# Optimization experiments

Hardware: AMD Instinct MI355X
Metric: run time of the kernel (lower is better)

## Reference

```python
import jax, jax.numpy as jnp
import numpy as np

B, S, D, H, F, E, K = 2, 2048, 1024, 16, 4096, 8, 2
EPS = 1e-6


def setup_inputs() -> dict:
    key = jax.random.key(0)
    ks = jax.random.split(key, 9)
    s = 0.02
    return {
        "x": jax.random.normal(ks[0], (B, S, D), jnp.float32),
        "n1_w": jnp.ones((D,), jnp.float32),
        "n2_w": jnp.ones((D,), jnp.float32),
        "wq": jax.random.normal(ks[1], (D, D), jnp.float32) * s,
        "wk": jax.random.normal(ks[2], (D, D), jnp.float32) * s,
        "wv": jax.random.normal(ks[3], (D, D), jnp.float32) * s,
        "wo": jax.random.normal(ks[4], (D, D), jnp.float32) * s,
        "router_w": jax.random.normal(ks[5], (E, D), jnp.float32) * s,  # nn.Linear(D, E, bias=False)
        "w1": jax.random.normal(ks[6], (E, D, F), jnp.float32) * s,
        "b1": jnp.zeros((E, F), jnp.float32),
        "w2": jax.random.normal(ks[7], (E, F, D), jnp.float32) * s,
        "b2": jnp.zeros((E, D), jnp.float32),
    }


def _rms(t, w):
    return t * w * jax.lax.rsqrt(jnp.mean(t * t, axis=-1, keepdims=True) + EPS)


def reference(x, n1_w, n2_w, wq, wk, wv, wo, router_w, w1, b1, w2, b2):
    hd = D // H
    # --- pre-norm causal multi-head self-attention ---
    h = _rms(x, n1_w)
    q = (h @ wq).reshape(B, S, H, hd)
    k = (h @ wk).reshape(B, S, H, hd)
    v = (h @ wv).reshape(B, S, H, hd)
    scores = jnp.einsum("bqhd,bkhd->bhqk", q, k) * (hd ** -0.5)
    causal = jnp.tril(jnp.ones((S, S), bool))
    scores = jnp.where(causal, scores, jnp.float32(-1e9))
    attn = jax.nn.softmax(scores, axis=-1)
    attn_out = jnp.einsum("bhqk,bkhd->bqhd", attn, v).reshape(B, S, D) @ wo
    x = x + attn_out
    # --- pre-norm MoE MLP: dense experts + top-k weighted combine ---
    h2 = _rms(x, n2_w)
    logits = h2 @ router_w.T                         # [B,S,E]
    probs = jax.nn.softmax(logits, axis=-1)
    topv, topi = jax.lax.top_k(probs, K)             # [B,S,K]
    topv = topv / jnp.sum(topv, axis=-1, keepdims=True)  # renormalized top-k gates
    bi = jnp.arange(B)[:, None, None]
    si = jnp.arange(S)[None, :, None]
    gates = jnp.zeros_like(probs).at[bi, si, topi].set(topv)  # sparse gates [B,S,E]
    eh = jax.nn.gelu(jnp.einsum("bsd,edf->ebsf", h2, w1) + b1[:, None, None, :])
    eo = jnp.einsum("ebsf,efd->ebsd", eh, w2) + b2[:, None, None, :]
    y = jnp.einsum("ebsd,bse->bsd", eo, gates)
    return x + y
```

## Files before the change

kernel.cpp:

```cpp
#include <hip/hip_runtime.h>
#include <hip/hip_bf16.h>


typedef float fx4 __attribute__((ext_vector_type(4)));
typedef short sx4 __attribute__((ext_vector_type(4)));
typedef short sx8 __attribute__((ext_vector_type(8)));
typedef int ix2 __attribute__((ext_vector_type(2)));
typedef int ix4 __attribute__((ext_vector_type(4)));

#define DEVFN static __device__ __forceinline__
#define MFMA16(a, b, c) __builtin_amdgcn_mfma_f32_16x16x32_bf16((a), (b), (c), 0, 0, 0)

typedef __attribute__((address_space(1))) const void GASV;
typedef __attribute__((address_space(3))) void LASV;

DEVFN short f2bf(float f) {
  unsigned u = __float_as_uint(f);
  return (short)((u + 0x7FFFu + ((u >> 16) & 1u)) >> 16);
}
DEVFN float bf2f(short s) { return __uint_as_float(((unsigned)(unsigned short)s) << 16); }

DEVFN int cvt_pk_bf16(float a, float b) {
  int r;
  asm("v_cvt_pk_bf16_f32 %0, %1, %2" : "=v"(r) : "v"(a), "v"(b));
  return r;
}

DEVFN void gll16(const short* g, short* l) {
  __builtin_amdgcn_global_load_lds((GASV*)g, (LASV*)l, 16, 0, 0);
}

DEVFN float fast_gelu(float x) {
  float u = 0.7978845608028654f * (x + 0.044715f * x * x * x);
  float e = __expf(2.0f * u);
  float t = 1.0f - 2.0f / (1.0f + e);
  return 0.5f * x * (1.0f + t);
}

DEVFN float wsum64(float v) {
#pragma unroll
  for (int m = 1; m < 64; m <<= 1) v += __shfl_xor(v, m);
  return v;
}

template <int SPLIT>
__global__ __launch_bounds__(256) void transpose_k(const float* in, short* oh, short* ol,
                                                   int R, int C) {
  __shared__ float t[64][65];
  const int c0 = blockIdx.x * 64, r0 = blockIdx.y * 64;
  const long long bofs = (long long)blockIdx.z * R * C;
  in += bofs;
  oh += bofs;
  if (SPLIT) ol += bofs;
  const int tid = threadIdx.x;
  const int rr = tid >> 4, cc4 = (tid & 15) * 4;
#pragma unroll
  for (int i = 0; i < 4; ++i) {
    int r = i * 16 + rr;
    fx4 v = *(const fx4*)(in + (long long)(r0 + r) * C + c0 + cc4);
    t[r][cc4] = v.x;
    t[r][cc4 + 1] = v.y;
    t[r][cc4 + 2] = v.z;
    t[r][cc4 + 3] = v.w;
  }
  __syncthreads();
#pragma unroll
  for (int i = 0; i < 4; ++i) {
    int oc = i * 16 + rr;
    sx4 hv, lv;
#pragma unroll
    for (int j = 0; j < 4; ++j) {
      float v = t[cc4 + j][oc];
      short hi = f2bf(v);
      hv[j] = hi;
      if (SPLIT) lv[j] = f2bf(v - bf2f(hi));
    }
    *(sx4*)(oh + (long long)(c0 + oc) * R + r0 + cc4) = hv;
    if (SPLIT) *(sx4*)(ol + (long long)(c0 + oc) * R + r0 + cc4) = lv;
  }
}

template <int SPLIT>
__global__ __launch_bounds__(256) void rms_k(const float* x, const float* w, short* hh,
                                             short* hl) {
  const int row = blockIdx.x, tid = threadIdx.x;
  const fx4 v = ((const fx4*)(x + (long long)row * 1024))[tid];
  float ss = v.x * v.x + v.y * v.y + v.z * v.z + v.w * v.w;
  ss = wsum64(ss);
  __shared__ float red[4];
  if ((tid & 63) == 0) red[tid >> 6] = ss;
  __syncthreads();
  ss = red[0] + red[1] + red[2] + red[3];
  const float rr = rsqrtf(ss * (1.0f / 1024.0f) + 1e-6f);
  const fx4 wv = ((const fx4*)w)[tid];
  float vals[4] = {v.x * wv.x * rr, v.y * wv.y * rr, v.z * wv.z * rr, v.w * wv.w * rr};
  sx4 oh, ol;
#pragma unroll
  for (int c = 0; c < 4; ++c) {
    short hi = f2bf(vals[c]);
    oh[c] = hi;
    if (SPLIT) ol[c] = f2bf(vals[c] - bf2f(hi));
  }
  ((sx4*)(hh + (long long)row * 1024))[tid] = oh;
  if (SPLIT) ((sx4*)(hl + (long long)row * 1024))[tid] = ol;
}

struct GemmArgs {
  const short *Ah, *Al, *Bh, *Bl;
  int K, lda, ldb, ldc;
  long long strideBe;
  short *out_h, *out_l;
  float* out_f;
  const float* resid;
  const float* bias;
  const int* tile_info;
  const int* n_tiles;
  const int* row_token;
  const float* row_gate;
};

template <int TERMS, int BK, int EPI>
__global__ __launch_bounds__(256) void gemm_k(GemmArgs a) {
  const int tid = threadIdx.x, lane = tid & 63, wave = tid >> 6;
  const int bx = blockIdx.x;
  int row0, expert = 0, valid = 128;
  if constexpr (EPI >= 3) {
    if ((int)blockIdx.y >= *a.n_tiles) return;
    const int* ti = a.tile_info + blockIdx.y * 4;
    expert = ti[0];
    row0 = ti[1];
    valid = ti[2];
  } else {
    row0 = blockIdx.y * 128;
  }
  const short* Bh = a.Bh + (EPI >= 3 ? (long long)expert * a.strideBe : 0ll);

  constexpr int CH = BK / 8;
  constexpr int SW = (BK == 64) ? 7 : 3;
  constexpr int NI = BK / 16;

  __shared__ short Ash[128 * BK];
  __shared__ short Bsh[128 * BK];
  __shared__ short Asl[TERMS == 3 ? 128 * BK : 1];
  __shared__ short Bsl[TERMS == 3 ? 128 * BK : 1];

  fx4 acc[4][4] = {};
  const int wr = wave >> 1, wc = wave & 1;

  for (int k0 = 0; k0 < a.K; k0 += BK) {
#pragma unroll
    for (int i = 0; i < NI; ++i) {
      int t = i * 256 + tid;
      int row = t / CH, c = t % CH;
      int cc = c ^ (row & SW);
      int lbase = (i * 256 + wave * 64) * 8;
      long long acol = k0 + cc * 8;
      gll16(a.Ah + (long long)(row0 + row) * a.lda + acol, &Ash[lbase]);
      gll16(Bh + (long long)(bx * 128 + row) * a.ldb + acol, &Bsh[lbase]);
      if constexpr (TERMS == 3) {
        gll16(a.Al + (long long)(row0 + row) * a.lda + acol, &Asl[lbase]);
        gll16(a.Bl + (long long)(bx * 128 + row) * a.ldb + acol, &Bsl[lbase]);
      }
    }
    __syncthreads();
#pragma unroll
    for (int kk = 0; kk < BK / 32; ++kk) {
      sx8 ah[4], bh[4], al_[4], bl_[4];
#pragma unroll
      for (int mi = 0; mi < 4; ++mi) {
        int row = wr * 64 + mi * 16 + (lane & 15);
        int sc = (kk * 4 + (lane >> 4)) ^ (row & SW);
        ah[mi] = *(const sx8*)&Ash[row * BK + sc * 8];
        if constexpr (TERMS == 3) al_[mi] = *(const sx8*)&Asl[row * BK + sc * 8];
      }
#pragma unroll
      for (int ni = 0; ni < 4; ++ni) {
        int row = wc * 64 + ni * 16 + (lane & 15);
        int sc = (kk * 4 + (lane >> 4)) ^ (row & SW);
        bh[ni] = *(const sx8*)&Bsh[row * BK + sc * 8];
        if constexpr (TERMS == 3) bl_[ni] = *(const sx8*)&Bsl[row * BK + sc * 8];
      }
#pragma unroll
      for (int mi = 0; mi < 4; ++mi)
#pragma unroll
        for (int ni = 0; ni < 4; ++ni) {
          acc[mi][ni] = MFMA16(ah[mi], bh[ni], acc[mi][ni]);
          if constexpr (TERMS == 3) {
            acc[mi][ni] = MFMA16(ah[mi], bl_[ni], acc[mi][ni]);
            acc[mi][ni] = MFMA16(al_[mi], bh[ni], acc[mi][ni]);
          }
        }
    }
    __syncthreads();
  }

#pragma unroll
  for (int mi = 0; mi < 4; ++mi)
#pragma unroll
    for (int ni = 0; ni < 4; ++ni) {
      fx4 v = acc[mi][ni];
      int rl = wr * 64 + mi * 16 + ((lane >> 4) << 2);
      int col = bx * 128 + wc * 64 + ni * 16 + (lane & 15);
#pragma unroll
      for (int j = 0; j < 4; ++j) {
        int r = rl + j;
        long long grow = (long long)row0 + r;
        float xv = v[j];
        if constexpr (EPI == 1) {
          short hi = f2bf(xv);
          a.out_h[grow * a.ldc + col] = hi;
          a.out_l[grow * a.ldc + col] = f2bf(xv - bf2f(hi));
        } else if constexpr (EPI == 2) {
          a.out_f[grow * a.ldc + col] = xv + a.resid[grow * a.ldc + col];
        } else if constexpr (EPI == 3) {
          xv += a.bias[expert * a.ldc + col];
          a.out_h[grow * a.ldc + col] = f2bf(fast_gelu(xv));
        } else if constexpr (EPI == 4) {
          if (r < valid) {
            xv += a.bias[expert * a.ldc + col];
            float g = a.row_gate[grow];
            int tok = a.row_token[grow];
            atomicAdd(&a.out_f[(long long)tok * 1024 + col], xv * g);
          }
        }
      }
    }
}

__global__ __launch_bounds__(128, 2) void flash_k(const short* __restrict__ qkv_h,
                                                  const short* __restrict__ qkv_l,
                                                  short* __restrict__ ao_h,
                                                  short* __restrict__ ao_l) {
  const int tid = threadIdx.x, lane = tid & 63, wave = tid >> 6;
  const int l15 = lane & 15, g = lane >> 4;
  const int qt = (blockIdx.x + blockIdx.y) & 31;
  const int bh = blockIdx.y;
  const int b = bh >> 4, h = bh & 15;
  const long long base = (long long)b * 2048 * 3072;
  const int qw = qt * 64 + wave * 32;

  __shared__ short Kh[4096], Kl[4096];
  __shared__ int VTh[64 * 34], VTl[64 * 34];

  sx8 qh[2][2], ql[2][2];
#pragma unroll
  for (int mb = 0; mb < 2; ++mb)
#pragma unroll
    for (int kk = 0; kk < 2; ++kk) {
      long long qofs =
          base + (long long)(qw + mb * 16 + l15) * 3072 + h * 64 + kk * 32 + g * 8;
      qh[mb][kk] = *(const sx8*)(qkv_h + qofs);
      ql[mb][kk] = *(const sx8*)(qkv_l + qofs);
    }

  fx4 o[2][4] = {};
  float m_r[2] = {-3e38f, -3e38f}, l_r[2] = {0.f, 0.f};

  const int krow0 = tid >> 3;
  const int kc8 = (tid & 7) * 8;
  const int kswz = ((tid & 7) ^ (krow0 & 7)) * 8;
  const int vu = tid >> 3;
  const int vd0 = (tid & 7) * 8;

  sx8 kr[4], krl[4], vr[4], vrl[4];

  auto load_tile = [&](int kt2) {
    const long long tb = base + (long long)(kt2 * 64) * 3072 + h * 64;
#pragma unroll
    for (int s = 0; s < 4; ++s) {
      long long gofs = tb + 1024 + (long long)(s * 16 + krow0) * 3072 + kc8;
      kr[s] = *(const sx8*)(qkv_h + gofs);
      krl[s] = *(const sx8*)(qkv_l + gofs);
    }
#pragma unroll
    for (int k4 = 0; k4 < 4; ++k4) {
      long long gofs = tb + 2048 + (long long)(4 * vu + k4) * 3072 + vd0;
      vr[k4] = *(const sx8*)(qkv_h + gofs);
      vrl[k4] = *(const sx8*)(qkv_l + gofs);
    }
  };

  const int nt = qt + 1;
  load_tile(0);

  for (int kt = 0; kt < nt; ++kt) {
#pragma unroll
    for (int s = 0; s < 4; ++s) {
      *(sx8*)&Kh[(s * 16 + krow0) * 64 + kswz] = kr[s];
      *(sx8*)&Kl[(s * 16 + krow0) * 64 + kswz] = krl[s];
    }
#pragma unroll
    for (int i = 0; i < 8; ++i) {
      int d = vd0 + i;
      ix2 wh, wl;
      wh[0] = (int)(unsigned short)vr[0][i] | ((int)(unsigned short)vr[1][i] << 16);
      wh[1] = (int)(unsigned short)vr[2][i] | ((int)(unsigned short)vr[3][i] << 16);
      wl[0] = (int)(unsigned short)vrl[0][i] | ((int)(unsigned short)vrl[1][i] << 16);
      wl[1] = (int)(unsigned short)vrl[2][i] | ((int)(unsigned short)vrl[3][i] << 16);
      *(ix2*)&VTh[d * 34 + 2 * vu] = wh;
      *(ix2*)&VTl[d * 34 + 2 * vu] = wl;
    }
    __syncthreads();

    if (kt + 1 < nt) load_tile(kt + 1);

    const bool diag = (kt == nt - 1);
    float pvv[2][16];
#pragma unroll
    for (int kc = 0; kc < 4; ++kc) {
      int row = kc * 16 + l15;
      int rsw = row & 7;
      fx4 s0 = {}, s1 = {};
#pragma unroll
      for (int kk = 0; kk < 2; ++kk) {
        int sc = ((kk * 4 + g) ^ rsw) * 8;
        sx8 khf = *(const sx8*)&Kh[row * 64 + sc];
        sx8 klf = *(const sx8*)&Kl[row * 64 + sc];
        s0 = MFMA16(khf, qh[0][kk], s0);
        s1 = MFMA16(khf, qh[1][kk], s1);
        s0 = MFMA16(khf, ql[0][kk], s0);
        s1 = MFMA16(khf, ql[1][kk], s1);
        s0 = MFMA16(klf, qh[0][kk], s0);
        s1 = MFMA16(klf, qh[1][kk], s1);
      }
#pragma unroll
      for (int j = 0; j < 4; ++j) {
        pvv[0][kc * 4 + j] = s0[j];
        pvv[1][kc * 4 + j] = s1[j];
      }
    }

    sx8 pah[2][2], pal[2][2];
#pragma unroll
    for (int mb = 0; mb < 2; ++mb) {
      const int qidx = qw + mb * 16 + l15;
      float t[16];
      float tmax = -3e38f;
#pragma unroll
      for (int i = 0; i < 16; ++i) {
        float sv = pvv[mb][i] * 0.18033688011112f;
        if (diag) {
          int key = kt * 64 + (i >> 2) * 16 + g * 4 + (i & 3);
          sv = (key > qidx) ? -3e38f : sv;
        }
        t[i] = sv;
        tmax = fmaxf(tmax, sv);
      }
      tmax = fmaxf(tmax, __shfl_xor(tmax, 16));
      tmax = fmaxf(tmax, __shfl_xor(tmax, 32));
      if (__any(tmax > m_r[mb] + 8.0f)) {
        float mnew = fmaxf(m_r[mb], tmax);
        float al = exp2f(m_r[mb] - mnew);
        l_r[mb] *= al;
        float aj[4];
#pragma unroll
        for (int j = 0; j < 4; ++j) aj[j] = __shfl(al, (lane & 48) | (g << 2) | j);
#pragma unroll
        for (int f = 0; f < 4; ++f)
#pragma unroll
          for (int j = 0; j < 4; ++j) o[mb][f][j] *= aj[j];
        m_r[mb] = mnew;
      }
      float ps = 0.f;
#pragma unroll
      for (int i = 0; i < 16; ++i) {
        float e = exp2f(t[i] - m_r[mb]);
        t[i] = e;
        ps += e;
      }
      l_r[mb] += ps;
#pragma unroll
      for (int grp = 0; grp < 2; ++grp) {
        ix4 ih, il;
#pragma unroll
        for (int q2 = 0; q2 < 4; ++q2) {
          float a = t[grp * 8 + 2 * q2], bb = t[grp * 8 + 2 * q2 + 1];
          int I = cvt_pk_bf16(a, bb);
          float h0 = __uint_as_float((unsigned)I << 16);
          float h1 = __uint_as_float((unsigned)I & 0xffff0000u);
          int L = cvt_pk_bf16(a - h0, bb - h1);
          ih[q2] = I;
          il[q2] = L;
        }
        pah[mb][grp] = __builtin_bit_cast(sx8, ih);
        pal[mb][grp] = __builtin_bit_cast(sx8, il);
      }
    }

    const ix2* vth = (const ix2*)VTh;
    const ix2* vtl = (const ix2*)VTl;
#pragma unroll
    for (int f = 0; f < 4; ++f) {
      int dd = f * 16 + l15;
      ix2 a0 = vth[dd * 17 + g], a1 = vth[dd * 17 + 4 + g];
      ix2 a2 = vth[dd * 17 + 8 + g], a3 = vth[dd * 17 + 12 + g];
      ix2 c0 = vtl[dd * 17 + g], c1 = vtl[dd * 17 + 4 + g];
      ix2 c2 = vtl[dd * 17 + 8 + g], c3 = vtl[dd * 17 + 12 + g];
      ix4 w;
      w[0] = a0[0]; w[1] = a0[1]; w[2] = a1[0]; w[3] = a1[1];
      sx8 vh8a = __builtin_bit_cast(sx8, w);
      w[0] = a2[0]; w[1] = a2[1]; w[2] = a3[0]; w[3] = a3[1];
      sx8 vh8b = __builtin_bit_cast(sx8, w);
      w[0] = c0[0]; w[1] = c0[1]; w[2] = c1[0]; w[3] = c1[1];
      sx8 vl8a = __builtin_bit_cast(sx8, w);
      w[0] = c2[0]; w[1] = c2[1]; w[2] = c3[0]; w[3] = c3[1];
      sx8 vl8b = __builtin_bit_cast(sx8, w);
#pragma unroll
      for (int mb = 0; mb < 2; ++mb) {
        o[mb][f] = MFMA16(pah[mb][0], vh8a, o[mb][f]);
        o[mb][f] = MFMA16(pah[mb][0], vl8a, o[mb][f]);
        o[mb][f] = MFMA16(pal[mb][0], vh8a, o[mb][f]);
        o[mb][f] = MFMA16(pah[mb][1], vh8b, o[mb][f]);
        o[mb][f] = MFMA16(pah[mb][1], vl8b, o[mb][f]);
        o[mb][f] = MFMA16(pal[mb][1], vh8b, o[mb][f]);
      }
    }
    __syncthreads();
  }

#pragma unroll
  for (int mb = 0; mb < 2; ++mb) {
    float lt = l_r[mb];
    lt += __shfl_xor(lt, 16);
    lt += __shfl_xor(lt, 32);
    float linv = 1.0f / lt;
    float lj[4];
#pragma unroll
    for (int j = 0; j < 4; ++j) lj[j] = __shfl(linv, (lane & 48) | (g << 2) | j);
#pragma unroll
    for (int f = 0; f < 4; ++f)
#pragma unroll
      for (int j = 0; j < 4; ++j) {
        float val = o[mb][f][j] * lj[j];
        long long orow = (long long)b * 2048 + qw + mb * 16 + g * 4 + j;
        int ocol = h * 64 + f * 16 + l15;
        short hi = f2bf(val);
        ao_h[orow * 1024 + ocol] = hi;
        ao_l[orow * 1024 + ocol] = f2bf(val - bf2f(hi));
      }
  }
}

__global__ __launch_bounds__(256) void router_k(const float* x2, const float* w,
                                                const float* rw, int* tok_e,
                                                float* tok_g) {
  const int tid = threadIdx.x, lane = tid & 63, wave = tid >> 6;
  const long long token = (long long)blockIdx.x * 4 + wave;
  const fx4* xr = (const fx4*)(x2 + token * 1024);
  const fx4* wr4 = (const fx4*)w;
  fx4 t[4];
  float ss = 0.0f;
#pragma unroll
  for (int i = 0; i < 4; ++i) {
    fx4 xv = xr[i * 64 + lane];
    fx4 wv = wr4[i * 64 + lane];
    ss += xv.x * xv.x + xv.y * xv.y + xv.z * xv.z + xv.w * xv.w;
    t[i].x = xv.x * wv.x;
    t[i].y = xv.y * wv.y;
    t[i].z = xv.z * wv.z;
    t[i].w = xv.w * wv.w;
  }
  ss = wsum64(ss);
  const float rr = rsqrtf(ss * (1.0f / 1024.0f) + 1e-6f);
  float logit[8];
#pragma unroll
  for (int e = 0; e < 8; ++e) {
    const fx4* re = (const fx4*)(rw + e * 1024);
    float acc = 0.0f;
#pragma unroll
    for (int i = 0; i < 4; ++i) {
      fx4 rv = re[i * 64 + lane];
      acc += t[i].x * rv.x + t[i].y * rv.y + t[i].z * rv.z + t[i].w * rv.w;
    }
    logit[e] = wsum64(acc) * rr;
  }
  float mx = logit[0];
#pragma unroll
  for (int e = 1; e < 8; ++e) mx = fmaxf(mx, logit[e]);
  float pe[8];
#pragma unroll
  for (int e = 0; e < 8; ++e) pe[e] = expf(logit[e] - mx);
  int e1 = 0;
  float b1v = pe[0];
#pragma unroll
  for (int e = 1; e < 8; ++e)
    if (pe[e] > b1v) {
      b1v = pe[e];
      e1 = e;
    }
  int e2 = -1;
  float b2v = -1.0f;
#pragma unroll
  for (int e = 0; e < 8; ++e)
    if (e != e1 && pe[e] > b2v) {
      b2v = pe[e];
      e2 = e;
    }
  if (lane == 0) {
    float inv = 1.0f / (b1v + b2v);
    tok_e[token * 2] = e1;
    tok_e[token * 2 + 1] = e2;
    tok_g[token * 2] = b1v * inv;
    tok_g[token * 2 + 1] = b2v * inv;
  }
}

__global__ __launch_bounds__(1024) void rank_k(const int* tok_e, const float* tok_g,
                                               int* tinfo, int* ntv, int* row_of_entry,
                                               int* row_token, float* row_gate) {
  const int tid = threadIdx.x, lane = tid & 63, wave = tid >> 6;
  __shared__ unsigned wtot[16][4];
  __shared__ unsigned woff[16][4];
  __shared__ int segsh[8];
  int e[8];
  {
    const int4* te = (const int4*)tok_e;
    int4 a = te[tid * 2], b = te[tid * 2 + 1];
    e[0] = a.x; e[1] = a.y; e[2] = a.z; e[3] = a.w;
    e[4] = b.x; e[5] = b.y; e[6] = b.z; e[7] = b.w;
  }
  unsigned c0 = 0, c1 = 0, c2 = 0, c3 = 0;
#pragma unroll
  for (int i = 0; i < 8; ++i) {
    unsigned f = 1u << ((e[i] & 1) << 4);
    int h = e[i] >> 1;
    c0 += (h == 0) ? f : 0u;
    c1 += (h == 1) ? f : 0u;
    c2 += (h == 2) ? f : 0u;
    c3 += (h == 3) ? f : 0u;
  }
  unsigned s0 = c0, s1 = c1, s2 = c2, s3 = c3;
#pragma unroll
  for (int d = 1; d < 64; d <<= 1) {
    unsigned t0 = __shfl_up(s0, d), t1 = __shfl_up(s1, d);
    unsigned t2 = __shfl_up(s2, d), t3 = __shfl_up(s3, d);
    if (lane >= d) { s0 += t0; s1 += t1; s2 += t2; s3 += t3; }
  }
  if (lane == 63) {
    wtot[wave][0] = s0; wtot[wave][1] = s1; wtot[wave][2] = s2; wtot[wave][3] = s3;
  }
  __syncthreads();
  if (wave == 0 && lane < 16) {
    unsigned v0 = wtot[lane][0], v1 = wtot[lane][1];
    unsigned v2 = wtot[lane][2], v3 = wtot[lane][3];
    unsigned i0 = v0, i1 = v1, i2 = v2, i3 = v3;
#pragma unroll
    for (int d = 1; d < 16; d <<= 1) {
      unsigned t0 = __shfl_up(i0, d), t1 = __shfl_up(i1, d);
      unsigned t2 = __shfl_up(i2, d), t3 = __shfl_up(i3, d);
      if (lane >= d) { i0 += t0; i1 += t1; i2 += t2; i3 += t3; }
    }
    woff[lane][0] = i0 - v0; woff[lane][1] = i1 - v1;
    woff[lane][2] = i2 - v2; woff[lane][3] = i3 - v3;
    if (lane == 15) {
      wtot[0][0] = i0; wtot[0][1] = i1; wtot[0][2] = i2; wtot[0][3] = i3;
    }
  }
  __syncthreads();
  if (tid == 0) {
    int off = 0, nt = 0;
    for (int ee = 0; ee < 8; ++ee) {
      unsigned tot = wtot[0][ee >> 1];
      int c = (int)((tot >> ((ee & 1) * 16)) & 0xFFFFu);
      segsh[ee] = off;
      int tt = (c + 127) >> 7;
      for (int i = 0; i < tt; ++i) {
        tinfo[nt * 4 + 0] = ee;
        tinfo[nt * 4 + 1] = off + i * 128;
        int v = c - i * 128;
        tinfo[nt * 4 + 2] = v > 128 ? 128 : v;
        tinfo[nt * 4 + 3] = 0;
        ++nt;
      }
      off += tt << 7;
    }
    *ntv = nt;
  }
  __syncthreads();
  unsigned x0 = woff[wave][0] + s0 - c0;
  unsigned x1 = woff[wave][1] + s1 - c1;
  unsigned x2 = woff[wave][2] + s2 - c2;
  unsigned x3 = woff[wave][3] + s3 - c3;
  const int entry0 = tid * 8;
#pragma unroll
  for (int i = 0; i < 8; ++i) {
    int ee = e[i];
    int h = ee >> 1, sh = (ee & 1) << 4;
    unsigned px = (h == 0) ? x0 : (h == 1) ? x1 : (h == 2) ? x2 : x3;
    int rank = (int)((px >> sh) & 0xFFFFu);
    unsigned f = 1u << sh;
    x0 += (h == 0) ? f : 0u;
    x1 += (h == 1) ? f : 0u;
    x2 += (h == 2) ? f : 0u;
    x3 += (h == 3) ? f : 0u;
    int row = segsh[ee] + rank;
    row_of_entry[entry0 + i] = row;
    row_token[row] = (entry0 + i) >> 1;
    row_gate[row] = tok_g[entry0 + i];
  }
}

__global__ __launch_bounds__(256) void gather_copy_k(const int* row_of_entry,
                                                     const short* h2, short* h2g) {
  const int tid = threadIdx.x, lane = tid & 63, wave = tid >> 6;
  const int entry = blockIdx.x * 4 + wave;
  const int token = entry >> 1;
  const int r = row_of_entry[entry];
  const sx8* src = (const sx8*)(h2 + (long long)token * 1024);
  sx8* dst = (sx8*)(h2g + (long long)r * 1024);
  dst[lane] = src[lane];
  dst[lane + 64] = src[lane + 64];
}

extern "C" void kernel_launch(void* const* d_in, const int* in_sizes, int n_in,
                              void* d_out, int out_size, void* d_ws, size_t ws_size,
                              hipStream_t stream) {
  (void)in_sizes;
  (void)n_in;
  (void)out_size;
  (void)ws_size;
  const float* x = (const float*)d_in[0];
  const float* n1w = (const float*)d_in[1];
  const float* n2w = (const float*)d_in[2];
  const float* wq = (const float*)d_in[3];
  const float* wk = (const float*)d_in[4];
  const float* wv = (const float*)d_in[5];
  const float* wo = (const float*)d_in[6];
  const float* rw = (const float*)d_in[7];
  const float* w1 = (const float*)d_in[8];
  const float* b1 = (const float*)d_in[9];
  const float* w2 = (const float*)d_in[10];
  const float* b2 = (const float*)d_in[11];
  float* out = (float*)d_out;
  char* ws = (char*)d_ws;

  short* wqkv_h = (short*)(ws + 0);
  short* wqkv_l = (short*)(ws + 6291456);
  short* wo_h = (short*)(ws + 12582912);
  short* wo_l = (short*)(ws + 14680064);
  short* h_h = (short*)(ws + 16777216);
  short* h_l = (short*)(ws + 25165824);
  short* qkv_h = (short*)(ws + 33554432);
  short* qkv_l = (short*)(ws + 58720256);
  short* ao_h = (short*)(ws + 83886080);
  short* ao_l = (short*)(ws + 92274688);
  short* h2 = (short*)(ws + 0);
  short* h2g = (short*)(ws + 8388608);
  short* wslot = (short*)(ws + 27262976);
  int* row_of_entry = (int*)(ws + 94371840);
  short* eh = (short*)(ws + 100663296);
  char* ctrl = ws + 176160768;
  int* ntv = (int*)(ctrl + 96);
  int* tinfo = (int*)(ctrl + 128);
  int* tok_e = (int*)(ctrl + 2048);
  float* tok_g = (float*)(ctrl + 2048 + 32768);
  int* row_token = (int*)(ctrl + 2048 + 65536);
  float* row_gate = (float*)(ctrl + 2048 + 65536 + 36864);

  transpose_k<1><<<dim3(16, 16, 1), 256, 0, stream>>>(wq, wqkv_h, wqkv_l, 1024, 1024);
  transpose_k<1><<<dim3(16, 16, 1), 256, 0, stream>>>(wk, wqkv_h + 1024 * 1024,
                                                      wqkv_l + 1024 * 1024, 1024, 1024);
  transpose_k<1><<<dim3(16, 16, 1), 256, 0, stream>>>(wv, wqkv_h + 2048 * 1024,
                                                      wqkv_l + 2048 * 1024, 1024, 1024);
  transpose_k<1><<<dim3(16, 16, 1), 256, 0, stream>>>(wo, wo_h, wo_l, 1024, 1024);

  rms_k<1><<<4096, 256, 0, stream>>>(x, n1w, h_h, h_l);

  {
    GemmArgs a = {};
    a.Ah = h_h;
    a.Al = h_l;
    a.Bh = wqkv_h;
    a.Bl = wqkv_l;
    a.K = 1024;
    a.lda = 1024;
    a.ldb = 1024;
    a.ldc = 3072;
    a.out_h = qkv_h;
    a.out_l = qkv_l;
    gemm_k<3, 32, 1><<<dim3(24, 32), 256, 0, stream>>>(a);
  }

  flash_k<<<dim3(32, 32), 128, 0, stream>>>(qkv_h, qkv_l, ao_h, ao_l);

  {
    GemmArgs a = {};
    a.Ah = ao_h;
    a.Al = ao_l;
    a.Bh = wo_h;
    a.Bl = wo_l;
    a.K = 1024;
    a.lda = 1024;
    a.ldb = 1024;
    a.ldc = 1024;
    a.out_f = out;
    a.resid = x;
    gemm_k<3, 32, 2><<<dim3(8, 32), 256, 0, stream>>>(a);
  }

  rms_k<0><<<4096, 256, 0, stream>>>(out, n2w, h2, nullptr);
  router_k<<<1024, 256, 0, stream>>>(out, n2w, rw, tok_e, tok_g);
  rank_k<<<1, 1024, 0, stream>>>(tok_e, tok_g, tinfo, ntv, row_of_entry, row_token,
                                 row_gate);
  gather_copy_k<<<2048, 256, 0, stream>>>(row_of_entry, h2, h2g);

  transpose_k<0><<<dim3(64, 16, 8), 256, 0, stream>>>(w1, wslot, nullptr, 1024, 4096);
  {
    GemmArgs a = {};
    a.Ah = h2g;
    a.Bh = wslot;
    a.K = 1024;
    a.lda = 1024;
    a.ldb = 1024;
    a.ldc = 4096;
    a.strideBe = (long long)4096 * 1024;
    a.out_h = eh;
    a.bias = b1;
    a.tile_info = tinfo;
    a.n_tiles = ntv;
    gemm_k<1, 64, 3><<<dim3(32, 80), 256, 0, stream>>>(a);
  }

  transpose_k<0><<<dim3(16, 64, 8), 256, 0, stream>>>(w2, wslot, nullptr, 4096, 1024);
  {
    GemmArgs a = {};
    a.Ah = eh;
    a.Bh = wslot;
    a.K = 4096;
    a.lda = 4096;
    a.ldb = 4096;
    a.ldc = 1024;
    a.strideBe = (long long)1024 * 4096;
    a.out_f = out;
    a.bias = b2;
    a.tile_info = tinfo;
    a.n_tiles = ntv;
    a.row_token = row_token;
    a.row_gate = row_gate;
    gemm_k<1, 64, 4><<<dim3(8, 80), 256, 0, stream>>>(a);
  }
}
```

Baseline: 673.2 us.

## Double-buffer GEMM LDS tiles, transpose MFMA output, vectorize epilogue, split-K second expert GEMM

The GEMM kernel now double-buffers its shared-memory A/B tiles, so the next K-slice loads while the current one is computed, and drops one barrier per iteration. MFMA operands are swapped so each lane holds four consecutive columns, which lets the epilogue issue vector stores and loads for the bf16 split, residual, bias and GELU paths. The second expert GEMM (K=4096) is split into two K halves over blockIdx.z. Both halves atomically accumulate into the output, and only the first adds the bias. In exchange, shared memory doubles, which may lower occupancy, and the split-K path doubles the atomic traffic.

Result: slower. 811.4 us (+20.5%).

```diff
diff --git a/kernel.cpp b/kernel.cpp
--- a/kernel.cpp
+++ b/kernel.cpp
@@ -122,6 +122,7 @@
 template <int TERMS, int BK, int EPI>
 __global__ __launch_bounds__(256) void gemm_k(GemmArgs a) {
   const int tid = threadIdx.x, lane = tid & 63, wave = tid >> 6;
+  const int l15 = lane & 15, g = lane >> 4;
   const int bx = blockIdx.x;
   int row0, expert = 0, valid = 128;
   if constexpr (EPI >= 3) {
@@ -133,98 +134,125 @@
   } else {
     row0 = blockIdx.y * 128;
   }
-  const short* Bh = a.Bh + (EPI >= 3 ? (long long)expert * a.strideBe : 0ll);
+  const short* Ap = a.Ah;
+  const short* Bp = a.Bh + (EPI >= 3 ? (long long)expert * a.strideBe : 0ll);
+  const int kbeg = blockIdx.z * a.K;
 
   constexpr int CH = BK / 8;
   constexpr int SW = (BK == 64) ? 7 : 3;
   constexpr int NI = BK / 16;
-
-  __shared__ short Ash[128 * BK];
-  __shared__ short Bsh[128 * BK];
-  __shared__ short Asl[TERMS == 3 ? 128 * BK : 1];
-  __shared__ short Bsl[TERMS == 3 ? 128 * BK : 1];
+  constexpr int TSZ = 128 * BK;
+
+  __shared__ short Ash[2][TSZ];
+  __shared__ short Bsh[2][TSZ];
+  __shared__ short Asl[TERMS == 3 ? 2 : 1][TERMS == 3 ? TSZ : 1];
+  __shared__ short Bsl[TERMS == 3 ? 2 : 1][TERMS == 3 ? TSZ : 1];
 
   fx4 acc[4][4] = {};
   const int wr = wave >> 1, wc = wave & 1;
 
-  for (int k0 = 0; k0 < a.K; k0 += BK) {
+  auto stage = [&](int s, int k0) {
 #pragma unroll
     for (int i = 0; i < NI; ++i) {
       int t = i * 256 + tid;
       int row = t / CH, c = t % CH;
       int cc = c ^ (row & SW);
       int lbase = (i * 256 + wave * 64) * 8;
-      long long acol = k0 + cc * 8;
-      gll16(a.Ah + (long long)(row0 + row) * a.lda + acol, &Ash[lbase]);
-      gll16(Bh + (long long)(bx * 128 + row) * a.ldb + acol, &Bsh[lbase]);
+      long long acol = kbeg + k0 + cc * 8;
+      gll16(Ap + (long long)(row0 + row) * a.lda + acol, &Ash[s][lbase]);
+      gll16(Bp + (long long)(bx * 128 + row) * a.ldb + acol, &Bsh[s][lbase]);
       if constexpr (TERMS == 3) {
-        gll16(a.Al + (long long)(row0 + row) * a.lda + acol, &Asl[lbase]);
-        gll16(a.Bl + (long long)(bx * 128 + row) * a.ldb + acol, &Bsl[lbase]);
-      }
-    }
-    __syncthreads();
+        gll16(a.Al + (long long)(row0 + row) * a.lda + acol, &Asl[s][lbase]);
+        gll16(a.Bl + (long long)(bx * 128 + row) * a.ldb + acol, &Bsl[s][lbase]);
+      }
+    }
+  };
+
+  auto compute = [&](int s) {
 #pragma unroll
     for (int kk = 0; kk < BK / 32; ++kk) {
       sx8 ah[4], bh[4], al_[4], bl_[4];
 #pragma unroll
       for (int mi = 0; mi < 4; ++mi) {
-        int row = wr * 64 + mi * 16 + (lane & 15);
-        int sc = (kk * 4 + (lane >> 4)) ^ (row & SW);
-        ah[mi] = *(const sx8*)&Ash[row * BK + sc * 8];
-        if constexpr (TERMS == 3) al_[mi] = *(const sx8*)&Asl[row * BK + sc * 8];
+        int row = wr * 64 + mi * 16 + l15;
+        int sc = (kk * 4 + g) ^ (row & SW);
+        ah[mi] = *(const sx8*)&Ash[s][row * BK + sc * 8];
+        if constexpr (TERMS == 3) al_[mi] = *(const sx8*)&Asl[s][row * BK + sc * 8];
       }
 #pragma unroll
       for (int ni = 0; ni < 4; ++ni) {
-        int row = wc * 64 + ni * 16 + (lane & 15);
-        int sc = (kk * 4 + (lane >> 4)) ^ (row & SW);
-        bh[ni] = *(const sx8*)&Bsh[row * BK + sc * 8];
-        if constexpr (TERMS == 3) bl_[ni] = *(const sx8*)&Bsl[row * BK + sc * 8];
+        int row = wc * 64 + ni * 16 + l15;
+        int sc = (kk * 4 + g) ^ (row & SW);
+        bh[ni] = *(const sx8*)&Bsh[s][row * BK + sc * 8];
+        if constexpr (TERMS == 3) bl_[ni] = *(const sx8*)&Bsl[s][row * BK + sc * 8];
       }
 #pragma unroll
       for (int mi = 0; mi < 4; ++mi)
 #pragma unroll
         for (int ni = 0; ni < 4; ++ni) {
-          acc[mi][ni] = MFMA16(ah[mi], bh[ni], acc[mi][ni]);
+          acc[mi][ni] = MFMA16(bh[ni], ah[mi], acc[mi][ni]);
           if constexpr (TERMS == 3) {
-            acc[mi][ni] = MFMA16(ah[mi], bl_[ni], acc[mi][ni]);
-            acc[mi][ni] = MFMA16(al_[mi], bh[ni], acc[mi][ni]);
+            acc[mi][ni] = MFMA16(bh[ni], al_[mi], acc[mi][ni]);
+            acc[mi][ni] = MFMA16(bl_[ni], ah[mi], acc[mi][ni]);
           }
         }
     }
-    __syncthreads();
-  }
-
-#pragma unroll
-  for (int mi = 0; mi < 4; ++mi)
+  };
+
+  const int NT = a.K / BK;
+  stage(0, 0);
+  __syncthreads();
+  for (int t = 0; t < NT; ++t) {
+    if (t + 1 < NT) stage((t + 1) & 1, (t + 1) * BK);
+    compute(t & 1);
+    if (t + 1 < NT) __syncthreads();
+  }
+
+#pragma unroll
+  for (int mi = 0; mi < 4; ++mi) {
+    const int m = wr * 64 + mi * 16 + l15;
+    const long long grow = (long long)row0 + m;
+    int tok = 0;
+    float gt = 0.f;
+    if constexpr (EPI == 4) {
+      if (m >= valid) continue;
+      tok = a.row_token[grow];
+      gt = a.row_gate[grow];
+    }
 #pragma unroll
     for (int ni = 0; ni < 4; ++ni) {
       fx4 v = acc[mi][ni];
-      int rl = wr * 64 + mi * 16 + ((lane >> 4) << 2);
-      int col = bx * 128 + wc * 64 + ni * 16 + (lane & 15);
-#pragma unroll
-      for (int j = 0; j < 4; ++j) {
-        int r = rl + j;
-        long long grow = (long long)row0 + r;
-        float xv = v[j];
-        if constexpr (EPI == 1) {
-          short hi = f2bf(xv);
-          a.out_h[grow * a.ldc + col] = hi;
-          a.out_l[grow * a.ldc + col] = f2bf(xv - bf2f(hi));
-        } else if constexpr (EPI == 2) {
-          a.out_f[grow * a.ldc + col] = xv + a.resid[grow * a.ldc + col];
-        } else if constexpr (EPI == 3) {
-          xv += a.bias[expert * a.ldc + col];
-          a.out_h[grow * a.ldc + col] = f2bf(fast_gelu(xv));
-        } else if constexpr (EPI == 4) {
-          if (r < valid) {
-            xv += a.bias[expert * a.ldc + col];
-            float g = a.row_gate[grow];
-            int tok = a.row_token[grow];
-            atomicAdd(&a.out_f[(long long)tok * 1024 + col], xv * g);
-          }
+      const int colb = bx * 128 + wc * 64 + ni * 16 + g * 4;
+      if constexpr (EPI == 1) {
+        sx4 hv, lv;
+#pragma unroll
+        for (int j = 0; j < 4; ++j) {
+          short hi = f2bf(v[j]);
+          hv[j] = hi;
+          lv[j] = f2bf(v[j] - bf2f(hi));
         }
-      }
-    }
+        *(sx4*)&a.out_h[grow * a.ldc + colb] = hv;
+        *(sx4*)&a.out_l[grow * a.ldc + colb] = lv;
+      } else if constexpr (EPI == 2) {
+        fx4 r = *(const fx4*)&a.resid[grow * a.ldc + colb];
+#pragma unroll
+        for (int j = 0; j < 4; ++j) v[j] += r[j];
+        *(fx4*)&a.out_f[grow * a.ldc + colb] = v;
+      } else if constexpr (EPI == 3) {
+        fx4 bb = *(const fx4*)&a.bias[expert * a.ldc + colb];
+        sx4 hv;
+#pragma unroll
+        for (int j = 0; j < 4; ++j) hv[j] = f2bf(fast_gelu(v[j] + bb[j]));
+        *(sx4*)&a.out_h[grow * a.ldc + colb] = hv;
+      } else {
+        fx4 bb = {0.f, 0.f, 0.f, 0.f};
+        if (blockIdx.z == 0) bb = *(const fx4*)&a.bias[expert * a.ldc + colb];
+#pragma unroll
+        for (int j = 0; j < 4; ++j)
+          atomicAdd(&a.out_f[(long long)tok * 1024 + colb + j], (v[j] + bb[j]) * gt);
+      }
+    }
+  }
 }
 
 __global__ __launch_bounds__(128, 2) void flash_k(const short* __restrict__ qkv_h,
@@ -726,7 +754,7 @@
     GemmArgs a = {};
     a.Ah = eh;
     a.Bh = wslot;
-    a.K = 4096;
+    a.K = 2048;
     a.lda = 4096;
     a.ldb = 4096;
     a.ldc = 1024;
@@ -737,6 +765,6 @@
     a.n_tiles = ntv;
     a.row_token = row_token;
     a.row_gate = row_gate;
-    gemm_k<1, 64, 4><<<dim3(8, 80), 256, 0, stream>>>(a);
-  }
-}
+    gemm_k<1, 64, 4><<<dim3(8, 80, 2), 256, 0, stream>>>(a);
+  }
+}
```

## Double-buffer attention GEMMs, swizzle workgroup order, replace MoE atomics with combine

Applied to the files above, without the earlier changes.

Adds a PIPE template flag so the QKV and output-projection GEMMs prefetch the next K tile into a second LDS buffer while computing the current one. All GEMM workgroups are remapped through an XCD-style interleave of the flat block index. The expert down-projection now writes gated bf16 rows to a buffer instead of doing float atomicAdd scatter, and a new combine kernel sums each token's two expert rows into the output. This trades atomic contention for an extra pass and bf16 rounding of expert outputs. Doubled LDS for the pipelined GEMMs may reduce occupancy.

New measurement: 752.0 us. +11.7%, slower.

```diff
diff --git a/kernel.cpp b/kernel.cpp
--- a/kernel.cpp
+++ b/kernel.cpp
@@ -115,39 +115,47 @@
   const float* bias;
   const int* tile_info;
   const int* n_tiles;
-  const int* row_token;
   const float* row_gate;
 };
 
-template <int TERMS, int BK, int EPI>
+template <int TERMS, int BK, int EPI, int PIPE>
 __global__ __launch_bounds__(256) void gemm_k(GemmArgs a) {
   const int tid = threadIdx.x, lane = tid & 63, wave = tid >> 6;
-  const int bx = blockIdx.x;
+  const int gx = gridDim.x;
+  const int nwg = gx * (int)gridDim.y;
+  int flat = (int)blockIdx.y * gx + (int)blockIdx.x;
+  flat = (flat & 7) * (nwg >> 3) + (flat >> 3);
+  const int bx = flat % gx;
+  const int by = flat / gx;
+
   int row0, expert = 0, valid = 128;
   if constexpr (EPI >= 3) {
-    if ((int)blockIdx.y >= *a.n_tiles) return;
-    const int* ti = a.tile_info + blockIdx.y * 4;
+    if (by >= *a.n_tiles) return;
+    const int* ti = a.tile_info + by * 4;
     expert = ti[0];
     row0 = ti[1];
     valid = ti[2];
   } else {
-    row0 = blockIdx.y * 128;
-  }
-  const short* Bh = a.Bh + (EPI >= 3 ? (long long)expert * a.strideBe : 0ll);
+    row0 = by * 128;
+  }
+  const short* Ap = a.Ah;
+  const short* Bp = a.Bh + (EPI >= 3 ? (long long)expert * a.strideBe : 0ll);
 
   constexpr int CH = BK / 8;
   constexpr int SW = (BK == 64) ? 7 : 3;
   constexpr int NI = BK / 16;
-
-  __shared__ short Ash[128 * BK];
-  __shared__ short Bsh[128 * BK];
-  __shared__ short Asl[TERMS == 3 ? 128 * BK : 1];
-  __shared__ short Bsl[TERMS == 3 ? 128 * BK : 1];
+  constexpr int TSZ = 128 * BK;
+  constexpr int NB = PIPE ? 2 : 1;
+
+  __shared__ short Ash[NB][TSZ];
+  __shared__ short Bsh[NB][TSZ];
+  __shared__ short Asl[TERMS == 3 ? NB : 1][TERMS == 3 ? TSZ : 1];
+  __shared__ short Bsl[TERMS == 3 ? NB : 1][TERMS == 3 ? TSZ : 1];
 
   fx4 acc[4][4] = {};
   const int wr = wave >> 1, wc = wave & 1;
 
-  for (int k0 = 0; k0 < a.K; k0 += BK) {
+  auto stage = [&](int s, int k0) {
 #pragma unroll
     for (int i = 0; i < NI; ++i) {
       int t = i * 256 + tid;
@@ -155,14 +163,16 @@
       int cc = c ^ (row & SW);
       int lbase = (i * 256 + wave * 64) * 8;
       long long acol = k0 + cc * 8;
-      gll16(a.Ah + (long long)(row0 + row) * a.lda + acol, &Ash[lbase]);
-      gll16(Bh + (long long)(bx * 128 + row) * a.ldb + acol, &Bsh[lbase]);
+      gll16(Ap + (long long)(row0 + row) * a.lda + acol, &Ash[s][lbase]);
+      gll16(Bp + (long long)(bx * 128 + row) * a.ldb + acol, &Bsh[s][lbase]);
       if constexpr (TERMS == 3) {
-        gll16(a.Al + (long long)(row0 + row) * a.lda + acol, &Asl[lbase]);
-        gll16(a.Bl + (long long)(bx * 128 + row) * a.ldb + acol, &Bsl[lbase]);
-      }
-    }
-    __syncthreads();
+        gll16(a.Al + (long long)(row0 + row) * a.lda + acol, &Asl[s][lbase]);
+        gll16(a.Bl + (long long)(bx * 128 + row) * a.ldb + acol, &Bsl[s][lbase]);
+      }
+    }
+  };
+
+  auto compute = [&](int s) {
 #pragma unroll
     for (int kk = 0; kk < BK / 32; ++kk) {
       sx8 ah[4], bh[4], al_[4], bl_[4];
@@ -170,15 +180,15 @@
       for (int mi = 0; mi < 4; ++mi) {
         int row = wr * 64 + mi * 16 + (lane & 15);
         int sc = (kk * 4 + (lane >> 4)) ^ (row & SW);
-        ah[mi] = *(const sx8*)&Ash[row * BK + sc * 8];
-        if constexpr (TERMS == 3) al_[mi] = *(const sx8*)&Asl[row * BK + sc * 8];
+        ah[mi] = *(const sx8*)&Ash[s][row * BK + sc * 8];
+        if constexpr (TERMS == 3) al_[mi] = *(const sx8*)&Asl[s][row * BK + sc * 8];
       }
 #pragma unroll
       for (int ni = 0; ni < 4; ++ni) {
         int row = wc * 64 + ni * 16 + (lane & 15);
         int sc = (kk * 4 + (lane >> 4)) ^ (row & SW);
-        bh[ni] = *(const sx8*)&Bsh[row * BK + sc * 8];
-        if constexpr (TERMS == 3) bl_[ni] = *(const sx8*)&Bsl[row * BK + sc * 8];
+        bh[ni] = *(const sx8*)&Bsh[s][row * BK + sc * 8];
+        if constexpr (TERMS == 3) bl_[ni] = *(const sx8*)&Bsl[s][row * BK + sc * 8];
       }
 #pragma unroll
       for (int mi = 0; mi < 4; ++mi)
@@ -191,7 +201,24 @@
           }
         }
     }
-    __syncthreads();
+  };
+
+  const int NT = a.K / BK;
+  stage(0, 0);
+  __syncthreads();
+  for (int t = 0; t < NT; ++t) {
+    if constexpr (PIPE) {
+      if (t + 1 < NT) stage((t + 1) & 1, (t + 1) * BK);
+      compute(t & 1);
+      if (t + 1 < NT) __syncthreads();
+    } else {
+      compute(0);
+      if (t + 1 < NT) {
+        __syncthreads();
+        stage(0, (t + 1) * BK);
+        __syncthreads();
+      }
+    }
   }
 
 #pragma unroll
@@ -215,16 +242,39 @@
         } else if constexpr (EPI == 3) {
           xv += a.bias[expert * a.ldc + col];
           a.out_h[grow * a.ldc + col] = f2bf(fast_gelu(xv));
-        } else if constexpr (EPI == 4) {
+        } else if constexpr (EPI == 5) {
           if (r < valid) {
             xv += a.bias[expert * a.ldc + col];
             float g = a.row_gate[grow];
-            int tok = a.row_token[grow];
-            atomicAdd(&a.out_f[(long long)tok * 1024 + col], xv * g);
+            a.out_h[grow * a.ldc + col] = f2bf(xv * g);
           }
         }
       }
     }
+}
+
+__global__ __launch_bounds__(256) void combine_k(const int* row_of_entry,
+                                                 const short* eo, float* out) {
+  const int tid = threadIdx.x, lane = tid & 63, wave = tid >> 6;
+  const long long token = (long long)blockIdx.x * 4 + wave;
+  const int r1 = row_of_entry[token * 2];
+  const int r2 = row_of_entry[token * 2 + 1];
+  const sx8* e1 = (const sx8*)(eo + (long long)r1 * 1024);
+  const sx8* e2 = (const sx8*)(eo + (long long)r2 * 1024);
+  float* op = out + token * 1024;
+#pragma unroll
+  for (int half = 0; half < 2; ++half) {
+    sx8 va = e1[lane + half * 64];
+    sx8 vb = e2[lane + half * 64];
+    int cb = (lane + half * 64) * 8;
+#pragma unroll
+    for (int q = 0; q < 2; ++q) {
+      fx4 o = *(const fx4*)(op + cb + q * 4);
+#pragma unroll
+      for (int j = 0; j < 4; ++j) o[j] += bf2f(va[q * 4 + j]) + bf2f(vb[q * 4 + j]);
+      *(fx4*)(op + cb + q * 4) = o;
+    }
+  }
 }
 
 __global__ __launch_bounds__(128, 2) void flash_k(const short* __restrict__ qkv_h,
@@ -646,6 +696,7 @@
   short* ao_l = (short*)(ws + 92274688);
   short* h2 = (short*)(ws + 0);
   short* h2g = (short*)(ws + 8388608);
+  short* eo = (short*)(ws + 8388608);
   short* wslot = (short*)(ws + 27262976);
   int* row_of_entry = (int*)(ws + 94371840);
   short* eh = (short*)(ws + 100663296);
@@ -678,7 +729,7 @@
     a.ldc = 3072;
     a.out_h = qkv_h;
     a.out_l = qkv_l;
-    gemm_k<3, 32, 1><<<dim3(24, 32), 256, 0, stream>>>(a);
+    gemm_k<3, 32, 1, 1><<<dim3(24, 32), 256, 0, stream>>>(a);
   }
 
   flash_k<<<dim3(32, 32), 128, 0, stream>>>(qkv_h, qkv_l, ao_h, ao_l);
@@ -695,7 +746,7 @@
     a.ldc = 1024;
     a.out_f = out;
     a.resid = x;
-    gemm_k<3, 32, 2><<<dim3(8, 32), 256, 0, stream>>>(a);
+    gemm_k<3, 32, 2, 1><<<dim3(8, 32), 256, 0, stream>>>(a);
   }
 
   rms_k<0><<<4096, 256, 0, stream>>>(out, n2w, h2, nullptr);
@@ -718,7 +769,7 @@
     a.bias = b1;
     a.tile_info = tinfo;
     a.n_tiles = ntv;
-    gemm_k<1, 64, 3><<<dim3(32, 80), 256, 0, stream>>>(a);
+    gemm_k<1, 64, 3, 0><<<dim3(32, 80), 256, 0, stream>>>(a);
   }
 
   transpose_k<0><<<dim3(16, 64, 8), 256, 0, stream>>>(w2, wslot, nullptr, 4096, 1024);
@@ -731,12 +782,13 @@
     a.ldb = 4096;
     a.ldc = 1024;
     a.strideBe = (long long)1024 * 4096;
-    a.out_f = out;
+    a.out_h = eo;
     a.bias = b2;
     a.tile_info = tinfo;
     a.n_tiles = ntv;
-    a.row_token = row_token;
     a.row_gate = row_gate;
-    gemm_k<1, 64, 4><<<dim3(8, 80), 256, 0, stream>>>(a);
-  }
-}
+    gemm_k<1, 64, 5, 0><<<dim3(8, 80), 256, 0, stream>>>(a);
+  }
+
+  combine_k<<<1024, 256, 0, stream>>>(row_of_entry, eo, out);
+}
```
